# Performance work log

Measured on AMD Instinct MI355X. Metric: run time of the kernel, lower is better.

## Reference

```python
import jax, jax.numpy as jnp
import numpy as np

M, A, N, Bb, RANK = 64, 64, 64, 64, 2  # d_in = N*Bb = 4096, d_out = M*A = 4096
TOKENS = 16384


def setup_inputs() -> dict:
    key = jax.random.key(0)
    k1, k2, k3, k4 = jax.random.split(key, 4)
    x = jax.random.normal(k1, (TOKENS, N * Bb), dtype=jnp.float32)
    btt_l = jax.random.normal(k2, (M, N * RANK, A), dtype=jnp.float32)
    btt_r = jax.random.normal(k3, (N, Bb, M * RANK), dtype=jnp.float32)
    bias = jax.random.normal(k4, (M * A,), dtype=jnp.float32)
    return {"x": x, "btt_l": btt_l, "btt_r": btt_r, "bias": bias}


def reference(x, btt_l, btt_r, bias):
    # Block tensor-train (BTT) factorized linear: y = BTT(btt_l, btt_r) @ x + bias
    B = x.shape[0]
    m, nr, a = btt_l.shape          # (M, N*RANK, A)
    n, b, mr = btt_r.shape          # (N, Bb, M*RANK)
    rank = nr // n
    # Stage 1: per n-block, map b -> m*rank
    h = jnp.einsum('tnb,nbk->tnk', x.reshape(B, n, b), btt_r)  # (B, n, m*rank)
    # Regroup: (B, n, m, rank) -> (B, m, n, rank) -> (B, m, n*rank)
    h = h.reshape(B, n, m, rank).transpose(0, 2, 1, 3).reshape(B, m, n * rank)
    # Stage 2: per m-block, map n*rank -> a
    y = jnp.einsum('tmj,mja->tma', h, btt_l).reshape(B, m * a)
    return y + bias
```

## Files before the change

kernel.cpp:

```cpp
#include <hip/hip_runtime.h>
#include <hip/hip_bf16.h>

typedef __attribute__((ext_vector_type(8))) short short8;
typedef __attribute__((ext_vector_type(4))) float f32x4;
typedef __attribute__((ext_vector_type(4))) unsigned int u32x4;
typedef __attribute__((ext_vector_type(2))) unsigned int u32x2;

#define DIN  4096
#define DOUT 4096
#define NTOK 16384

static __device__ __forceinline__ unsigned short f2b(float f) {
  union { __hip_bfloat16 h; unsigned short u; } cv;
  cv.h = __float2bfloat16(f);
  return cv.u;
}

__global__ __launch_bounds__(256) void prep_r(const float* __restrict__ r,
                                              unsigned short* __restrict__ rt) {
  __shared__ unsigned short tile[64 * 132];
  const int n = blockIdx.x;
  const int q = threadIdx.x;
#pragma unroll
  for (int it = 0; it < 8; ++it) {
    const int idx = q + it * 256;
    const int b = idx >> 5, k4 = idx & 31;
    const float4 v = *(const float4*)(r + (size_t)n * 8192 + b * 128 + k4 * 4);
    unsigned int lo = (unsigned)f2b(v.x) | ((unsigned)f2b(v.y) << 16);
    unsigned int hi = (unsigned)f2b(v.z) | ((unsigned)f2b(v.w) << 16);
    u32x2 pk = {lo, hi};
    *(u32x2*)((char*)tile + (b * 264 + k4 * 8)) = pk;
  }
  __syncthreads();
#pragma unroll
  for (int it = 0; it < 32; ++it) {
    const int o = q + it * 256;
    const int c = o >> 6, b = o & 63;
    rt[(size_t)n * 8192 + o] = tile[b * 132 + c];
  }
}

__global__ __launch_bounds__(256) void prep_l(const float* __restrict__ l,
                                              unsigned short* __restrict__ lt) {
  __shared__ unsigned short tile[128 * 68];
  const int m = blockIdx.x;
  const int q = threadIdx.x;
#pragma unroll
  for (int it = 0; it < 8; ++it) {
    const int idx = q + it * 256;
    const int j = idx >> 4, a4 = idx & 15;
    const float4 v = *(const float4*)(l + (size_t)m * 8192 + j * 64 + a4 * 4);
    unsigned int lo = (unsigned)f2b(v.x) | ((unsigned)f2b(v.y) << 16);
    unsigned int hi = (unsigned)f2b(v.z) | ((unsigned)f2b(v.w) << 16);
    u32x2 pk = {lo, hi};
    *(u32x2*)((char*)tile + (j * 136 + a4 * 8)) = pk;
  }
  __syncthreads();
#pragma unroll
  for (int it = 0; it < 32; ++it) {
    const int o = q + it * 256;
    const int a = o >> 7, j = o & 127;
    lt[(size_t)m * 8192 + o] = tile[j * 68 + a];
  }
}

__global__ __launch_bounds__(512) void k1(const float* __restrict__ x,
                                          const unsigned short* __restrict__ rt,
                                          unsigned short* __restrict__ hbuf,
                                          int tok0) {
  __shared__ unsigned short xs[32 * 64];
  __shared__ unsigned short rs[128 * 64];
  const int bid = blockIdx.x;
  const int tb = bid >> 2, ns = bid & 3;
  const int tid = threadIdx.x;
  const int wave = tid >> 6, lane = tid & 63;
  const int l15 = lane & 15, l4 = lane >> 4;
  const int t0 = tok0 + tb * 32;

  const int xr = tid >> 4, xc4 = tid & 15;
  const int xbyte = xr * 128 + ((xc4 * 8) ^ ((xr & 7) << 4));
  const int sw = (l15 & 7) << 4;
  const int ccol = wave * 16 + l15;

  for (int ni = 0; ni < 16; ++ni) {
    const int n = ns * 16 + ni;
    __syncthreads();
    {
      const float4 v = *(const float4*)(x + (size_t)(t0 + xr) * DIN + n * 64 + xc4 * 4);
      unsigned int lo = (unsigned)f2b(v.x) | ((unsigned)f2b(v.y) << 16);
      unsigned int hi = (unsigned)f2b(v.z) | ((unsigned)f2b(v.w) << 16);
      u32x2 pk = {lo, hi};
      *(u32x2*)((char*)xs + xbyte) = pk;
    }
#pragma unroll
    for (int it = 0; it < 2; ++it) {
      const int q = tid + it * 512;
      const int rr = q >> 3, rsl = q & 7;
      u32x4 v = *(const u32x4*)(rt + (size_t)n * 8192 + rr * 64 + rsl * 8);
      *(u32x4*)((char*)rs + (rr * 128 + ((rsl * 16) ^ ((rr & 7) << 4)))) = v;
    }
    __syncthreads();

    f32x4 acc0 = {0.f, 0.f, 0.f, 0.f};
    f32x4 acc1 = {0.f, 0.f, 0.f, 0.f};
#pragma unroll
    for (int ks = 0; ks < 2; ++ks) {
      const int kb = ks * 64 + l4 * 16;
      short8 a0 = *(const short8*)((char*)xs + ((l15) * 128 + (kb ^ sw)));
      short8 a1 = *(const short8*)((char*)xs + ((16 + l15) * 128 + (kb ^ sw)));
      short8 bv = *(const short8*)((char*)rs + (ccol * 128 + (kb ^ ((ccol & 7) << 4))));
      acc0 = __builtin_amdgcn_mfma_f32_16x16x32_bf16(a0, bv, acc0, 0, 0, 0);
      acc1 = __builtin_amdgcn_mfma_f32_16x16x32_bf16(a1, bv, acc1, 0, 0, 0);
    }
    const int tii0 = l4 * 4;
#pragma unroll
    for (int mt = 0; mt < 2; ++mt) {
      const f32x4 a = mt ? acc1 : acc0;
      unsigned int lo = (unsigned)f2b(a[0]) | ((unsigned)f2b(a[1]) << 16);
      unsigned int hi = (unsigned)f2b(a[2]) | ((unsigned)f2b(a[3]) << 16);
      u32x2 pk = {lo, hi};
      const int tioG = tb * 2 + mt;
      unsigned short* dst = hbuf + (((size_t)(tioG * 64 + n) * 128 + ccol) * 16 + tii0);
      *(u32x2*)dst = pk;
    }
  }
}

__global__ __launch_bounds__(512) void k2(const unsigned short* __restrict__ hbuf,
                                          const unsigned short* __restrict__ lt,
                                          const float* __restrict__ bias,
                                          float* __restrict__ y,
                                          int tok0) {
  __shared__ unsigned short as_[32 * 128];
  __shared__ unsigned short ls[64 * 128];
  const int bid = blockIdx.x;
  const int tb = bid >> 2, ms = bid & 3;
  const int tid = threadIdx.x;
  const int wave = tid >> 6, lane = tid & 63;
  const int l15 = lane & 15, l4 = lane >> 4;
  const int wr = wave >> 2, wc = wave & 3;

  const int hh = tid & 1, nr = (tid >> 1) & 127, tio_l = tid >> 8;
  const int nn = nr >> 1, r2 = nr & 1;

  const int ta = wr * 16 + l15;
  const int aa = wc * 16 + l15;
  const int swt = (ta & 7) << 4;
  const int swa = (aa & 7) << 4;

  for (int mi = 0; mi < 16; ++mi) {
    const int m = ms * 16 + mi;
    __syncthreads();
    {
      const unsigned short* src =
          hbuf + (((size_t)((tb * 2 + tio_l) * 64 + nn) * 128 + (m * 2 + r2)) * 16 + hh * 8);
      u32x4 v = *(const u32x4*)src;
#pragma unroll
      for (int e = 0; e < 8; ++e) {
        const unsigned int wrd = v[e >> 1];
        const unsigned short val = (e & 1) ? (unsigned short)(wrd >> 16)
                                           : (unsigned short)(wrd & 0xffff);
        const int t = tio_l * 16 + hh * 8 + e;
        *(unsigned short*)((char*)as_ + (t * 256 + ((nr * 2) ^ ((t & 7) << 4)))) = val;
      }
    }
#pragma unroll
    for (int it = 0; it < 2; ++it) {
      const int q2 = tid + it * 512;
      const int ar = q2 >> 4, sl = q2 & 15;
      u32x4 v = *(const u32x4*)(lt + (size_t)m * 8192 + ar * 128 + sl * 8);
      *(u32x4*)((char*)ls + (ar * 256 + ((sl * 16) ^ ((ar & 7) << 4)))) = v;
    }
    __syncthreads();

    f32x4 acc = {0.f, 0.f, 0.f, 0.f};
#pragma unroll
    for (int ks = 0; ks < 4; ++ks) {
      const int kb = ks * 64 + l4 * 16;
      short8 av = *(const short8*)((char*)as_ + (ta * 256 + (kb ^ swt)));
      short8 bv = *(const short8*)((char*)ls + (aa * 256 + (kb ^ swa)));
      acc = __builtin_amdgcn_mfma_f32_16x16x32_bf16(av, bv, acc, 0, 0, 0);
    }
    const float bvv = bias[m * 64 + aa];
    const int tg0 = tok0 + tb * 32 + wr * 16 + l4 * 4;
#pragma unroll
    for (int jj = 0; jj < 4; ++jj) {
      y[(size_t)(tg0 + jj) * DOUT + m * 64 + aa] = acc[jj] + bvv;
    }
  }
}

extern "C" void kernel_launch(void* const* d_in, const int* in_sizes, int n_in,
                              void* d_out, int out_size, void* d_ws, size_t ws_size,
                              hipStream_t stream) {
  const float* x    = (const float*)d_in[0];
  const float* bl   = (const float*)d_in[1];
  const float* br   = (const float*)d_in[2];
  const float* bias = (const float*)d_in[3];
  float* y = (float*)d_out;

  unsigned short* rt   = (unsigned short*)d_ws;
  unsigned short* ltw  = rt + 64 * 8192;
  unsigned short* hbuf = ltw + 64 * 8192;

  size_t fixed = (size_t)2 * 64 * 8192 * 2;
  int chunk = 4096;
  while (chunk > 512 && fixed + (size_t)chunk * 8192 * 2 > ws_size) chunk >>= 1;
  const int nchunk = NTOK / chunk;
  const int grid = (chunk / 32) * 4;

  prep_r<<<64, 256, 0, stream>>>(br, rt);
  prep_l<<<64, 256, 0, stream>>>(bl, ltw);
  for (int c = 0; c < nchunk; ++c) {
    k1<<<grid, 512, 0, stream>>>(x, rt, hbuf, c * chunk);
    k2<<<grid, 512, 0, stream>>>(hbuf, ltw, bias, y, c * chunk);
  }
}
```

Baseline: 265.5 us.

## Keep BTT weight fragments in registers and double-buffer stage-2 LDS staging

Restructures both BTT stages so each block handles one n (or m) block across a 256-token strip. The weight fragments are loaded once into registers instead of being restaged through LDS for every token tile. Stage 1 now reads x directly into MFMA operands with no LDS or barriers. Stage 2 double-buffers the transposed hidden tile so the next tile's staging overlaps the current MFMAs. The two weight-prep kernels are merged into one launch, and the chunk size may now drop to 256 tokens. The cost is higher register pressure and a different hbuf indexing scheme that must stay consistent between k1 and k2.

Result: slower. 298.9 us (+12.6%).

```diff
diff --git a/kernel.cpp b/kernel.cpp
--- a/kernel.cpp
+++ b/kernel.cpp
@@ -16,177 +16,167 @@
   return cv.u;
 }
 
-__global__ __launch_bounds__(256) void prep_r(const float* __restrict__ r,
-                                              unsigned short* __restrict__ rt) {
-  __shared__ unsigned short tile[64 * 132];
-  const int n = blockIdx.x;
+static __device__ __forceinline__ short8 pack8(float4 f0, float4 f1) {
+  short8 s;
+  s[0] = (short)f2b(f0.x); s[1] = (short)f2b(f0.y);
+  s[2] = (short)f2b(f0.z); s[3] = (short)f2b(f0.w);
+  s[4] = (short)f2b(f1.x); s[5] = (short)f2b(f1.y);
+  s[6] = (short)f2b(f1.z); s[7] = (short)f2b(f1.w);
+  return s;
+}
+
+__global__ __launch_bounds__(256) void prep(const float* __restrict__ r,
+                                            const float* __restrict__ l,
+                                            unsigned short* __restrict__ rt,
+                                            unsigned short* __restrict__ lt) {
+  __shared__ unsigned short tile[128 * 68];
   const int q = threadIdx.x;
-#pragma unroll
-  for (int it = 0; it < 8; ++it) {
-    const int idx = q + it * 256;
-    const int b = idx >> 5, k4 = idx & 31;
-    const float4 v = *(const float4*)(r + (size_t)n * 8192 + b * 128 + k4 * 4);
-    unsigned int lo = (unsigned)f2b(v.x) | ((unsigned)f2b(v.y) << 16);
-    unsigned int hi = (unsigned)f2b(v.z) | ((unsigned)f2b(v.w) << 16);
-    u32x2 pk = {lo, hi};
-    *(u32x2*)((char*)tile + (b * 264 + k4 * 8)) = pk;
-  }
-  __syncthreads();
-#pragma unroll
-  for (int it = 0; it < 32; ++it) {
-    const int o = q + it * 256;
-    const int c = o >> 6, b = o & 63;
-    rt[(size_t)n * 8192 + o] = tile[b * 132 + c];
-  }
-}
-
-__global__ __launch_bounds__(256) void prep_l(const float* __restrict__ l,
-                                              unsigned short* __restrict__ lt) {
-  __shared__ unsigned short tile[128 * 68];
-  const int m = blockIdx.x;
-  const int q = threadIdx.x;
-#pragma unroll
-  for (int it = 0; it < 8; ++it) {
-    const int idx = q + it * 256;
-    const int j = idx >> 4, a4 = idx & 15;
-    const float4 v = *(const float4*)(l + (size_t)m * 8192 + j * 64 + a4 * 4);
-    unsigned int lo = (unsigned)f2b(v.x) | ((unsigned)f2b(v.y) << 16);
-    unsigned int hi = (unsigned)f2b(v.z) | ((unsigned)f2b(v.w) << 16);
-    u32x2 pk = {lo, hi};
-    *(u32x2*)((char*)tile + (j * 136 + a4 * 8)) = pk;
-  }
-  __syncthreads();
-#pragma unroll
-  for (int it = 0; it < 32; ++it) {
-    const int o = q + it * 256;
-    const int a = o >> 7, j = o & 127;
-    lt[(size_t)m * 8192 + o] = tile[j * 68 + a];
-  }
-}
-
-__global__ __launch_bounds__(512) void k1(const float* __restrict__ x,
+  if (blockIdx.x < 64) {
+    const int n = blockIdx.x;
+#pragma unroll
+    for (int it = 0; it < 8; ++it) {
+      const int idx = q + it * 256;
+      const int b = idx >> 5, k4 = idx & 31;
+      const float4 v = *(const float4*)(r + (size_t)n * 8192 + b * 128 + k4 * 4);
+      unsigned int lo = (unsigned)f2b(v.x) | ((unsigned)f2b(v.y) << 16);
+      unsigned int hi = (unsigned)f2b(v.z) | ((unsigned)f2b(v.w) << 16);
+      u32x2 pk = {lo, hi};
+      *(u32x2*)((char*)tile + (b * 264 + k4 * 8)) = pk;
+    }
+    __syncthreads();
+#pragma unroll
+    for (int it = 0; it < 32; ++it) {
+      const int o = q + it * 256;
+      const int c = o >> 6, b = o & 63;
+      rt[(size_t)n * 8192 + o] = tile[b * 132 + c];
+    }
+  } else {
+    const int m = blockIdx.x - 64;
+#pragma unroll
+    for (int it = 0; it < 8; ++it) {
+      const int idx = q + it * 256;
+      const int j = idx >> 4, a4 = idx & 15;
+      const float4 v = *(const float4*)(l + (size_t)m * 8192 + j * 64 + a4 * 4);
+      unsigned int lo = (unsigned)f2b(v.x) | ((unsigned)f2b(v.y) << 16);
+      unsigned int hi = (unsigned)f2b(v.z) | ((unsigned)f2b(v.w) << 16);
+      u32x2 pk = {lo, hi};
+      *(u32x2*)((char*)tile + (j * 136 + a4 * 8)) = pk;
+    }
+    __syncthreads();
+#pragma unroll
+    for (int it = 0; it < 32; ++it) {
+      const int o = q + it * 256;
+      const int a = o >> 7, j = o & 127;
+      lt[(size_t)m * 8192 + o] = tile[j * 68 + a];
+    }
+  }
+}
+
+__global__ __launch_bounds__(256) void k1(const float* __restrict__ x,
                                           const unsigned short* __restrict__ rt,
                                           unsigned short* __restrict__ hbuf,
                                           int tok0) {
-  __shared__ unsigned short xs[32 * 64];
-  __shared__ unsigned short rs[128 * 64];
-  const int bid = blockIdx.x;
-  const int tb = bid >> 2, ns = bid & 3;
-  const int tid = threadIdx.x;
-  const int wave = tid >> 6, lane = tid & 63;
+  const int n = blockIdx.y;
+  const int strip = blockIdx.x;
+  const int wave = threadIdx.x >> 6, lane = threadIdx.x & 63;
   const int l15 = lane & 15, l4 = lane >> 4;
-  const int t0 = tok0 + tb * 32;
-
-  const int xr = tid >> 4, xc4 = tid & 15;
-  const int xbyte = xr * 128 + ((xc4 * 8) ^ ((xr & 7) << 4));
-  const int sw = (l15 & 7) << 4;
-  const int ccol = wave * 16 + l15;
-
-  for (int ni = 0; ni < 16; ++ni) {
-    const int n = ns * 16 + ni;
-    __syncthreads();
-    {
-      const float4 v = *(const float4*)(x + (size_t)(t0 + xr) * DIN + n * 64 + xc4 * 4);
-      unsigned int lo = (unsigned)f2b(v.x) | ((unsigned)f2b(v.y) << 16);
-      unsigned int hi = (unsigned)f2b(v.z) | ((unsigned)f2b(v.w) << 16);
+
+  short8 bf[8][2];
+  {
+    const unsigned short* rbase = rt + (size_t)n * 8192 + l15 * 64 + l4 * 8;
+#pragma unroll
+    for (int ct = 0; ct < 8; ++ct)
+#pragma unroll
+      for (int ks = 0; ks < 2; ++ks)
+        bf[ct][ks] = *(const short8*)(rbase + ct * 1024 + ks * 32);
+  }
+
+  for (int tt = 0; tt < 4; ++tt) {
+    const int tile = strip * 16 + tt * 4 + wave;
+    const float* xr = x + (size_t)(tok0 + tile * 16 + l15) * DIN + n * 64 + l4 * 8;
+    const float4 f0 = *(const float4*)(xr);
+    const float4 f1 = *(const float4*)(xr + 4);
+    const float4 g0 = *(const float4*)(xr + 32);
+    const float4 g1 = *(const float4*)(xr + 36);
+    const short8 a0 = pack8(f0, f1);
+    const short8 a1 = pack8(g0, g1);
+    unsigned short* hb = hbuf + (size_t)(tile * 64 + n) * 2048 + l15 * 16 + l4 * 4;
+#pragma unroll
+    for (int ct = 0; ct < 8; ++ct) {
+      f32x4 acc = {0.f, 0.f, 0.f, 0.f};
+      acc = __builtin_amdgcn_mfma_f32_16x16x32_bf16(a0, bf[ct][0], acc, 0, 0, 0);
+      acc = __builtin_amdgcn_mfma_f32_16x16x32_bf16(a1, bf[ct][1], acc, 0, 0, 0);
+      unsigned int lo = (unsigned)f2b(acc[0]) | ((unsigned)f2b(acc[1]) << 16);
+      unsigned int hi = (unsigned)f2b(acc[2]) | ((unsigned)f2b(acc[3]) << 16);
       u32x2 pk = {lo, hi};
-      *(u32x2*)((char*)xs + xbyte) = pk;
-    }
-#pragma unroll
-    for (int it = 0; it < 2; ++it) {
-      const int q = tid + it * 512;
-      const int rr = q >> 3, rsl = q & 7;
-      u32x4 v = *(const u32x4*)(rt + (size_t)n * 8192 + rr * 64 + rsl * 8);
-      *(u32x4*)((char*)rs + (rr * 128 + ((rsl * 16) ^ ((rr & 7) << 4)))) = v;
-    }
-    __syncthreads();
-
-    f32x4 acc0 = {0.f, 0.f, 0.f, 0.f};
-    f32x4 acc1 = {0.f, 0.f, 0.f, 0.f};
-#pragma unroll
-    for (int ks = 0; ks < 2; ++ks) {
-      const int kb = ks * 64 + l4 * 16;
-      short8 a0 = *(const short8*)((char*)xs + ((l15) * 128 + (kb ^ sw)));
-      short8 a1 = *(const short8*)((char*)xs + ((16 + l15) * 128 + (kb ^ sw)));
-      short8 bv = *(const short8*)((char*)rs + (ccol * 128 + (kb ^ ((ccol & 7) << 4))));
-      acc0 = __builtin_amdgcn_mfma_f32_16x16x32_bf16(a0, bv, acc0, 0, 0, 0);
-      acc1 = __builtin_amdgcn_mfma_f32_16x16x32_bf16(a1, bv, acc1, 0, 0, 0);
-    }
-    const int tii0 = l4 * 4;
-#pragma unroll
-    for (int mt = 0; mt < 2; ++mt) {
-      const f32x4 a = mt ? acc1 : acc0;
-      unsigned int lo = (unsigned)f2b(a[0]) | ((unsigned)f2b(a[1]) << 16);
-      unsigned int hi = (unsigned)f2b(a[2]) | ((unsigned)f2b(a[3]) << 16);
-      u32x2 pk = {lo, hi};
-      const int tioG = tb * 2 + mt;
-      unsigned short* dst = hbuf + (((size_t)(tioG * 64 + n) * 128 + ccol) * 16 + tii0);
-      *(u32x2*)dst = pk;
-    }
-  }
-}
-
-__global__ __launch_bounds__(512) void k2(const unsigned short* __restrict__ hbuf,
+      *(u32x2*)(hb + ct * 256) = pk;
+    }
+  }
+}
+
+__global__ __launch_bounds__(256) void k2(const unsigned short* __restrict__ hbuf,
                                           const unsigned short* __restrict__ lt,
                                           const float* __restrict__ bias,
                                           float* __restrict__ y,
                                           int tok0) {
-  __shared__ unsigned short as_[32 * 128];
-  __shared__ unsigned short ls[64 * 128];
-  const int bid = blockIdx.x;
-  const int tb = bid >> 2, ms = bid & 3;
+  __shared__ unsigned short as_[2][32 * 128];
+  const int m = blockIdx.y;
+  const int strip = blockIdx.x;
   const int tid = threadIdx.x;
   const int wave = tid >> 6, lane = tid & 63;
   const int l15 = lane & 15, l4 = lane >> 4;
-  const int wr = wave >> 2, wc = wave & 3;
-
-  const int hh = tid & 1, nr = (tid >> 1) & 127, tio_l = tid >> 8;
-  const int nn = nr >> 1, r2 = nr & 1;
-
-  const int ta = wr * 16 + l15;
-  const int aa = wc * 16 + l15;
-  const int swt = (ta & 7) << 4;
-  const int swa = (aa & 7) << 4;
-
-  for (int mi = 0; mi < 16; ++mi) {
-    const int m = ms * 16 + mi;
+
+  short8 bfr[4];
+  {
+    const unsigned short* lbase = lt + (size_t)m * 8192 + (wave * 16 + l15) * 128 + l4 * 8;
+#pragma unroll
+    for (int ks = 0; ks < 4; ++ks) bfr[ks] = *(const short8*)(lbase + ks * 32);
+  }
+  const int acol = wave * 16 + l15;
+  const float bv = bias[m * 64 + acol];
+
+  auto stage = [&](int it, int b) {
+#pragma unroll
+    for (int half = 0; half < 2; ++half) {
+      const int idx = tid + half * 256;
+      const int hh = idx & 1, nr = (idx >> 1) & 127, tio = idx >> 8;
+      const int nn = nr >> 1, r2 = nr & 1;
+      const int tg16 = strip * 16 + it * 2 + tio;
+      const u32x4 v = *(const u32x4*)(hbuf + (size_t)(tg16 * 64 + nn) * 2048 +
+                                      (m * 2 + r2) * 16 + hh * 8);
+#pragma unroll
+      for (int e = 0; e < 8; ++e) {
+        const unsigned int w = v[e >> 1];
+        const unsigned short val = (e & 1) ? (unsigned short)(w >> 16)
+                                           : (unsigned short)(w & 0xffff);
+        const int t = tio * 16 + hh * 8 + e;
+        *(unsigned short*)((char*)as_[b] + (t * 256 + ((nr * 2) ^ ((t & 7) << 4)))) = val;
+      }
+    }
+  };
+
+  stage(0, 0);
+  __syncthreads();
+  int buf = 0;
+  for (int it = 0; it < 8; ++it) {
+    if (it + 1 < 8) stage(it + 1, buf ^ 1);
+#pragma unroll
+    for (int th = 0; th < 2; ++th) {
+      const int ta = th * 16 + l15;
+      f32x4 acc = {0.f, 0.f, 0.f, 0.f};
+#pragma unroll
+      for (int ks = 0; ks < 4; ++ks) {
+        const short8 av = *(const short8*)((char*)as_[buf] +
+                            (ta * 256 + ((ks * 64 + l4 * 16) ^ ((ta & 7) << 4))));
+        acc = __builtin_amdgcn_mfma_f32_16x16x32_bf16(av, bfr[ks], acc, 0, 0, 0);
+      }
+      const size_t t0 = (size_t)(tok0 + strip * 256 + it * 32 + th * 16 + l4 * 4);
+#pragma unroll
+      for (int jj = 0; jj < 4; ++jj)
+        y[(t0 + jj) * DOUT + m * 64 + acol] = acc[jj] + bv;
+    }
     __syncthreads();
-    {
-      const unsigned short* src =
-          hbuf + (((size_t)((tb * 2 + tio_l) * 64 + nn) * 128 + (m * 2 + r2)) * 16 + hh * 8);
-      u32x4 v = *(const u32x4*)src;
-#pragma unroll
-      for (int e = 0; e < 8; ++e) {
-        const unsigned int wrd = v[e >> 1];
-        const unsigned short val = (e & 1) ? (unsigned short)(wrd >> 16)
-                                           : (unsigned short)(wrd & 0xffff);
-        const int t = tio_l * 16 + hh * 8 + e;
-        *(unsigned short*)((char*)as_ + (t * 256 + ((nr * 2) ^ ((t & 7) << 4)))) = val;
-      }
-    }
-#pragma unroll
-    for (int it = 0; it < 2; ++it) {
-      const int q2 = tid + it * 512;
-      const int ar = q2 >> 4, sl = q2 & 15;
-      u32x4 v = *(const u32x4*)(lt + (size_t)m * 8192 + ar * 128 + sl * 8);
-      *(u32x4*)((char*)ls + (ar * 256 + ((sl * 16) ^ ((ar & 7) << 4)))) = v;
-    }
-    __syncthreads();
-
-    f32x4 acc = {0.f, 0.f, 0.f, 0.f};
-#pragma unroll
-    for (int ks = 0; ks < 4; ++ks) {
-      const int kb = ks * 64 + l4 * 16;
-      short8 av = *(const short8*)((char*)as_ + (ta * 256 + (kb ^ swt)));
-      short8 bv = *(const short8*)((char*)ls + (aa * 256 + (kb ^ swa)));
-      acc = __builtin_amdgcn_mfma_f32_16x16x32_bf16(av, bv, acc, 0, 0, 0);
-    }
-    const float bvv = bias[m * 64 + aa];
-    const int tg0 = tok0 + tb * 32 + wr * 16 + l4 * 4;
-#pragma unroll
-    for (int jj = 0; jj < 4; ++jj) {
-      y[(size_t)(tg0 + jj) * DOUT + m * 64 + aa] = acc[jj] + bvv;
-    }
+    buf ^= 1;
   }
 }
 
@@ -203,16 +193,15 @@
   unsigned short* ltw  = rt + 64 * 8192;
   unsigned short* hbuf = ltw + 64 * 8192;
 
-  size_t fixed = (size_t)2 * 64 * 8192 * 2;
+  const size_t fixed = (size_t)2 * 64 * 8192 * 2;
   int chunk = 4096;
-  while (chunk > 512 && fixed + (size_t)chunk * 8192 * 2 > ws_size) chunk >>= 1;
+  while (chunk > 256 && fixed + (size_t)chunk * 8192 * 2 > ws_size) chunk >>= 1;
   const int nchunk = NTOK / chunk;
-  const int grid = (chunk / 32) * 4;
-
-  prep_r<<<64, 256, 0, stream>>>(br, rt);
-  prep_l<<<64, 256, 0, stream>>>(bl, ltw);
+  const int strips = chunk / 256;
+
+  prep<<<128, 256, 0, stream>>>(br, bl, rt, ltw);
   for (int c = 0; c < nchunk; ++c) {
-    k1<<<grid, 512, 0, stream>>>(x, rt, hbuf, c * chunk);
-    k2<<<grid, 512, 0, stream>>>(hbuf, ltw, bias, y, c * chunk);
-  }
-}
+    k1<<<dim3(strips, 64), 256, 0, stream>>>(x, rt, hbuf, c * chunk);
+    k2<<<dim3(strips, 64), 256, 0, stream>>>(hbuf, ltw, bias, y, c * chunk);
+  }
+}
```
